# Kernel tuning notes

Hardware: AMD Instinct MI355X
Metric: run time of the kernel (lower is better)

## Reference

```python
import jax, jax.numpy as jnp
import numpy as np

N_USERS = 60000
N_ITEMS = 40000
N_NODES = N_USERS + N_ITEMS
N_EDGES = 1_000_000
D = 64
BN_EPS = 1e-3  # tf.layers.batch_normalization default epsilon


def setup_inputs() -> dict:
    key = jax.random.key(0)
    ks = jax.random.split(key, 16)
    s = 1.0 / np.sqrt(D)  # uniform-ish init scale for [D,D] weights
    w = lambda k: (jax.random.uniform(k, (D, D), jnp.float32, -1.0, 1.0) * s)
    return {
        "u_features": jax.random.normal(ks[0], (N_USERS, D), jnp.float32),
        "v_features": jax.random.normal(ks[1], (N_ITEMS, D), jnp.float32),
        "edge_start": jax.random.randint(ks[2], (N_EDGES,), 0, N_NODES, jnp.int32),
        "edge_end": jax.random.randint(ks[3], (N_EDGES,), 0, N_NODES, jnp.int32),
        "Ui1": w(ks[4]), "Uj1": w(ks[5]), "Vi1": w(ks[6]), "Vj1": w(ks[7]),
        "bu1": jnp.zeros((D,), jnp.float32), "bv1": jnp.zeros((D,), jnp.float32),
        "Ui2": w(ks[8]), "Uj2": w(ks[9]), "Vi2": w(ks[10]), "Vj2": w(ks[11]),
        "bu2": jnp.zeros((D,), jnp.float32), "bv2": jnp.zeros((D,), jnp.float32),
        "R": w(ks[12]),
        "gamma1": jnp.ones((D,), jnp.float32), "beta1": jnp.zeros((D,), jnp.float32),
        "gamma2": jnp.ones((D,), jnp.float32), "beta2": jnp.zeros((D,), jnp.float32),
    }


def _stage(x, Ui, Uj, Vi, Vj, bu, bv, e_start, e_end, n_nodes):
    # gate = sigmoid(E_end@(x Vi) + E_start@(x Vj) + bv)   -> edge gather
    gate = jax.nn.sigmoid((x @ Vi)[e_end] + (x @ Vj)[e_start] + bv)  # [E, D]
    msg = gate * (x @ Ui)[e_start]                                    # [E, D]
    # x Uj + E_end.T @ msg + bu   -> scatter-add to destination nodes
    agg = jax.ops.segment_sum(msg, e_end, num_segments=n_nodes)       # [N, D]
    return x @ Uj + agg + bu


def _batchnorm(x, gamma, beta):
    mean = jnp.mean(x, axis=0)
    var = jnp.var(x, axis=0)
    return gamma * (x - mean) * jax.lax.rsqrt(var + BN_EPS) + beta


def reference(u_features, v_features, edge_start, edge_end,
              Ui1, Uj1, Vi1, Vj1, bu1, bv1,
              Ui2, Uj2, Vi2, Vj2, bu2, bv2,
              R, gamma1, beta1, gamma2, beta2):
    num_users = u_features.shape[0]
    x_in = jnp.concatenate([u_features, v_features], axis=0)  # [N, D]
    n = x_in.shape[0]
    x = _stage(x_in, Ui1, Uj1, Vi1, Vj1, bu1, bv1, edge_start, edge_end, n)
    x = jax.nn.relu(_batchnorm(x, gamma1, beta1))
    x = _stage(x, Ui2, Uj2, Vi2, Vj2, bu2, bv2, edge_start, edge_end, n)
    x = _batchnorm(x, gamma2, beta2)
    x = jax.nn.relu(x + x_in @ R)  # residual branch
    return x[:num_users], x[num_users:]
```

## Files before the change

kernel.cpp:

```cpp
#include <hip/hip_runtime.h>
#include <hip/hip_bf16.h>

#define NUSERS 60000
#define NNODES 100000
#define DD 64
#define NGB 1563
#define GMM 782
#define NBUK 196
#define ESB 2048
#define NBH 400

typedef __hip_bfloat16 bf16;
using bf16x8 = __attribute__((ext_vector_type(8))) short;
using f32x4  = __attribute__((ext_vector_type(4))) float;

__device__ __forceinline__ float b2f(bf16 x) { return __bfloat162float(x); }
__device__ __forceinline__ bf16 f2b(float x) { return __float2bfloat16(x); }
__device__ __forceinline__ unsigned short fbits(float x) {
    union { bf16 b; unsigned short u; } cv; cv.b = f2b(x); return cv.u;
}
__device__ __forceinline__ float us2f(unsigned short h) {
    union { unsigned u; float f; } t; t.u = (unsigned)h << 16; return t.f;
}
__device__ __forceinline__ float lo_bf16(unsigned w) {
    union { unsigned u; float f; } t; t.u = w << 16; return t.f;
}
__device__ __forceinline__ float hi_bf16(unsigned w) {
    union { unsigned u; float f; } t; t.u = w & 0xFFFF0000u; return t.f;
}
__device__ __forceinline__ float ldf(const void* p, size_t i, int isbf) {
    if (isbf) return b2f(((const bf16*)p)[i]);
    return ((const float*)p)[i];
}
__device__ __forceinline__ unsigned pack2(float a, float b) {
    return (unsigned)fbits(a) | ((unsigned)fbits(b) << 16);
}
__device__ __forceinline__ unsigned pr2(float x0, float x1, float a0, float a1,
                                        float b0, float b1) {
    float t0 = a0 * x0 + b0, t1 = a1 * x1 + b1;
    t0 = t0 > 0.f ? t0 : 0.f;
    t1 = t1 > 0.f ? t1 : 0.f;
    return pack2(t0, t1);
}

__global__ __launch_bounds__(256) void k_bhist(
    const int* __restrict__ ee, const unsigned short* __restrict__ hsn,
    int* __restrict__ flag, int* __restrict__ bh, int E)
{
    __shared__ int h[256];
    int t = threadIdx.x;
    if (blockIdx.x == 0) {
        int cnt = 0;
        for (int i = t; i < 1024; i += 256) {
            int e = (hsn[2 * i] >> 7) & 0xFF;
            cnt += (e >= 100 && e <= 140) ? 1 : 0;
        }
        h[t] = cnt;
        __syncthreads();
        for (int s = 128; s > 0; s >>= 1) {
            if (t < s) h[t] += h[t + s];
            __syncthreads();
        }
        if (t == 0) flag[0] = (h[0] > 512) ? 1 : 0;
        __syncthreads();
    }
    h[t] = 0;
    __syncthreads();
    for (int e = blockIdx.x * 256 + t; e < E; e += gridDim.x * 256)
        atomicAdd(&h[ee[e] >> 9], 1);
    __syncthreads();
    bh[blockIdx.x * 256 + t] = h[t];
}

__global__ void k_bscan(const int* __restrict__ bh, int* __restrict__ bbase,
                        int* __restrict__ bcursor, float* __restrict__ redz)
{
    __shared__ int sd[256];
    int t = threadIdx.x;
    int v = 0;
    for (int b = 0; b < NBH; b++) v += bh[b * 256 + t];
    sd[t] = v;
    __syncthreads();
    for (int off = 1; off < 256; off <<= 1) {
        int x = (t >= off) ? sd[t - off] : 0;
        __syncthreads();
        sd[t] += x;
        __syncthreads();
    }
    int excl = sd[t] - v;
    bbase[t] = excl;
    bcursor[t] = excl;
    for (int i = t; i < 4096; i += 256) redz[i] = 0.f;
}

__global__ __launch_bounds__(256) void k_bscatter(
    const int* __restrict__ es, const int* __restrict__ ee,
    int* __restrict__ bcursor, unsigned* __restrict__ ebuf, int E)
{
    __shared__ int h[256], gb[256], lr[256];
    int t = threadIdx.x;
    h[t] = 0;
    lr[t] = 0;
    __syncthreads();
    int base = blockIdx.x * ESB;
    unsigned ent[8];
    int bk[8];
#pragma unroll
    for (int i = 0; i < 8; i++) {
        int e = base + t + i * 256;
        if (e < E) {
            int s = es[e], d = ee[e];
            bk[i] = d >> 9;
            ent[i] = (unsigned)s | ((unsigned)(d & 511) << 20);
            atomicAdd(&h[bk[i]], 1);
        } else bk[i] = -1;
    }
    __syncthreads();
    if (h[t]) gb[t] = atomicAdd(&bcursor[t], h[t]);
    __syncthreads();
#pragma unroll
    for (int i = 0; i < 8; i++) {
        if (bk[i] >= 0) {
            int r = atomicAdd(&lr[bk[i]], 1);
            ebuf[gb[bk[i]] + r] = ent[i];
        }
    }
}

__global__ __launch_bounds__(256) void k_group(
    const int* __restrict__ bbase, const unsigned* __restrict__ ebuf,
    int* __restrict__ rowptr, int* __restrict__ srcidx)
{
    __shared__ int h[512], sc[512];
    int b = blockIdx.x, t = threadIdx.x;
    int lo = bbase[b], hi = bbase[b + 1];
    h[t] = 0;
    h[t + 256] = 0;
    __syncthreads();
    for (int i = lo + t; i < hi; i += 256)
        atomicAdd(&h[ebuf[i] >> 20], 1);
    __syncthreads();
    sc[t] = h[t];
    sc[t + 256] = h[t + 256];
    __syncthreads();
    for (int off = 1; off < 512; off <<= 1) {
        int v0 = (t >= off) ? sc[t - off] : 0;
        int v1 = (t + 256 >= off) ? sc[t + 256 - off] : 0;
        __syncthreads();
        sc[t] += v0;
        sc[t + 256] += v1;
        __syncthreads();
    }
    int n0 = b * 512 + t, n1 = b * 512 + t + 256;
    int e0 = lo + sc[t] - h[t];
    int e1 = lo + sc[t + 256] - h[t + 256];
    if (n0 < NNODES) rowptr[n0] = e0;
    if (n1 < NNODES) rowptr[n1] = e1;
    if (b == NBUK - 1 && t == 0) rowptr[NNODES] = hi;
    h[t] = e0;
    h[t + 256] = e1;
    __syncthreads();
    for (int i = lo + t; i < hi; i += 256) {
        unsigned en = ebuf[i];
        int pos = atomicAdd(&h[en >> 20], 1);
        int s = (int)(en & 0xFFFFF);
        srcidx[pos] = s < NNODES ? s : 0;
    }
}

template <int MODE>
__device__ __forceinline__ void stage_load(
    int tile, int tid, int bfflag,
    const void* u, const void* v, const unsigned short* Aacc,
    const float* ab, uint4& w0, uint4& w1)
{
    int r = tid >> 2, c0 = (tid & 3) * 16;
    int row = tile * DD + r;
    int rowc = row < NNODES ? row : NNODES - 1;
    if (MODE == 0) {
        const void* src = (rowc < NUSERS) ? u : v;
        size_t off = (rowc < NUSERS) ? ((size_t)rowc * DD + c0)
                                     : ((size_t)(rowc - NUSERS) * DD + c0);
        if (bfflag) {
            const uint4* p = (const uint4*)((const unsigned short*)src + off);
            w0 = p[0];
            w1 = p[1];
        } else {
            const float4* p = (const float4*)((const float*)src + off);
            float4 f0 = p[0], f1 = p[1], f2 = p[2], f3 = p[3];
            w0 = make_uint4(pack2(f0.x, f0.y), pack2(f0.z, f0.w),
                            pack2(f1.x, f1.y), pack2(f1.z, f1.w));
            w1 = make_uint4(pack2(f2.x, f2.y), pack2(f2.z, f2.w),
                            pack2(f3.x, f3.y), pack2(f3.z, f3.w));
        }
    } else {
        const uint4* p = (const uint4*)(Aacc + (size_t)rowc * DD + c0);
        unsigned aw[8];
        *(uint4*)&aw[0] = p[0];
        *(uint4*)&aw[4] = p[1];
        const float4* pa = (const float4*)(ab + c0);
        const float4* pb = (const float4*)(ab + 64 + c0);
        float av[16], bv[16];
#pragma unroll
        for (int j = 0; j < 4; j++) {
            float4 fa = pa[j], fb = pb[j];
            av[4 * j] = fa.x; av[4 * j + 1] = fa.y;
            av[4 * j + 2] = fa.z; av[4 * j + 3] = fa.w;
            bv[4 * j] = fb.x; bv[4 * j + 1] = fb.y;
            bv[4 * j + 2] = fb.z; bv[4 * j + 3] = fb.w;
        }
        unsigned ow[8];
#pragma unroll
        for (int j = 0; j < 8; j++)
            ow[j] = pr2(lo_bf16(aw[j]), hi_bf16(aw[j]),
                        av[2 * j], av[2 * j + 1], bv[2 * j], bv[2 * j + 1]);
        w0 = *(uint4*)&ow[0];
        w1 = *(uint4*)&ow[4];
    }
}

__device__ __forceinline__ void stage_store(unsigned short* xbuf, int tid,
                                            const uint4& w0, const uint4& w1)
{
    int r = tid >> 2, c0 = (tid & 3) * 16;
    *(uint4*)&xbuf[r * 72 + c0] = w0;
    *((uint4*)&xbuf[r * 72 + c0] + 1) = w1;
}

template <int MODE>
__global__ __launch_bounds__(256, 4) void k_mm4_mfma(
    const void* __restrict__ u, const void* __restrict__ v,
    const float* __restrict__ red, const void* __restrict__ gm,
    const void* __restrict__ bt,
    const void* __restrict__ W0, const void* __restrict__ W1,
    const void* __restrict__ W2, const void* __restrict__ W3,
    const void* __restrict__ b0, const void* __restrict__ b1,
    const int* __restrict__ flag,
    unsigned short* __restrict__ A, unsigned short* __restrict__ Ed,
    unsigned* __restrict__ Tw)
{
    __shared__ __align__(16) unsigned short lsd[4 * DD * 72];
    __shared__ __align__(16) float abs_s[128];
    const int bfflag = flag[0];
    const int tid = threadIdx.x;

    if (MODE == 1) {
        if (tid < 64) {
            float sm = 0.f, sq = 0.f;
#pragma unroll
            for (int s = 0; s < 8; s++) {
                sm += red[s * 256 + tid];
                sq += red[s * 256 + 128 + tid];
            }
            float mean = sm * (1.f / NNODES);
            float var = sq * (1.f / NNODES) - mean * mean;
            float a = ldf(gm, tid, bfflag) * rsqrtf(var + 1e-3f);
            abs_s[tid] = a;
            abs_s[64 + tid] = ldf(bt, tid, bfflag) - mean * a;
        }
        __syncthreads();
    }

    int t = blockIdx.x;
    uint4 xa, xb;
    stage_load<MODE>(t, tid, bfflag, u, v, A, abs_s, xa, xb);

    if (bfflag) {
#define WSTG_BF(m, src)                                                   \
        _Pragma("unroll")                                                 \
        for (int j = 0; j < 2; j++) {                                     \
            int i = tid + j * 256; int e0 = i * 8;                        \
            *(uint4*)&lsd[(m) * 4608 + (e0 >> 6) * 72 + (e0 & 63)] =      \
                ((const uint4*)(src))[i];                                 \
        }
        WSTG_BF(0, W0) WSTG_BF(1, W1) WSTG_BF(2, W2) WSTG_BF(3, W3)
    } else {
#define WSTG_F32(m, src)                                                  \
        _Pragma("unroll")                                                 \
        for (int j = 0; j < 4; j++) {                                     \
            int i = tid + j * 256; int e0 = i * 4;                        \
            float4 f = ((const float4*)(src))[i];                         \
            *(uint2*)&lsd[(m) * 4608 + (e0 >> 6) * 72 + (e0 & 63)] =      \
                make_uint2(pack2(f.x, f.y), pack2(f.z, f.w));             \
        }
        WSTG_F32(0, W0) WSTG_F32(1, W1) WSTG_F32(2, W2) WSTG_F32(3, W3)
    }
    __syncthreads();

    const int wv = tid >> 6, lane = tid & 63;
    const int quad = lane >> 4, ln = lane & 15;
    const int mA = (wv < 2) ? wv : 2;
    bf16x8 bfrA[2][4], bfrB[2][4];
#pragma unroll
    for (int ks = 0; ks < 2; ks++)
#pragma unroll
        for (int nt = 0; nt < 4; nt++)
#pragma unroll
            for (int j = 0; j < 8; j++)
                bfrA[ks][nt][j] = (short)lsd[mA * 4608 +
                    (ks * 32 + quad * 8 + j) * 72 + nt * 16 + ln];
    if (wv >= 2) {
#pragma unroll
        for (int ks = 0; ks < 2; ks++)
#pragma unroll
            for (int nt = 0; nt < 4; nt++)
#pragma unroll
                for (int j = 0; j < 8; j++)
                    bfrB[ks][nt][j] = (short)lsd[3 * 4608 +
                        (ks * 32 + quad * 8 + j) * 72 + nt * 16 + ln];
    }
    float bias[4];
#pragma unroll
    for (int nt = 0; nt < 4; nt++)
        bias[nt] = (wv == 0) ? ldf(b0, nt * 16 + ln, bfflag)
                 : (wv == 1) ? ldf(b1, nt * 16 + ln, bfflag) : 0.f;
    __syncthreads();

    auto compute = [&](const unsigned short* xt, int row0) {
        if (wv < 2) {
#pragma unroll
            for (int rt = 0; rt < 4; rt++) {
                int m = rt * 16 + ln;
                bf16x8 af0 = *(const bf16x8*)&xt[m * 72 + quad * 8];
                bf16x8 af1 = *(const bf16x8*)&xt[m * 72 + 32 + quad * 8];
#pragma unroll
                for (int nt = 0; nt < 4; nt++) {
                    f32x4 c = {0.f, 0.f, 0.f, 0.f};
                    c = __builtin_amdgcn_mfma_f32_16x16x32_bf16(af0, bfrA[0][nt], c, 0, 0, 0);
                    c = __builtin_amdgcn_mfma_f32_16x16x32_bf16(af1, bfrA[1][nt], c, 0, 0, 0);
                    int col = nt * 16 + ln;
#pragma unroll
                    for (int r = 0; r < 4; r++) {
                        int row = row0 + rt * 16 + quad * 4 + r;
                        if (row < NNODES) {
                            size_t o = (size_t)row * DD + col;
                            if (wv == 0) A[o] = fbits(c[r] + bias[nt]);
                            else         Ed[o] = fbits(__expf(-(c[r] + bias[nt])));
                        }
                    }
                }
            }
        } else {
            const int rtb = (wv - 2) * 2;
#pragma unroll
            for (int rr = 0; rr < 2; rr++) {
                int rt = rtb + rr;
                int m = rt * 16 + ln;
                bf16x8 af0 = *(const bf16x8*)&xt[m * 72 + quad * 8];
                bf16x8 af1 = *(const bf16x8*)&xt[m * 72 + 32 + quad * 8];
#pragma unroll
                for (int nt = 0; nt < 4; nt++) {
                    f32x4 c2 = {0.f, 0.f, 0.f, 0.f};
                    f32x4 c3 = {0.f, 0.f, 0.f, 0.f};
                    c2 = __builtin_amdgcn_mfma_f32_16x16x32_bf16(af0, bfrA[0][nt], c2, 0, 0, 0);
                    c2 = __builtin_amdgcn_mfma_f32_16x16x32_bf16(af1, bfrA[1][nt], c2, 0, 0, 0);
                    c3 = __builtin_amdgcn_mfma_f32_16x16x32_bf16(af0, bfrB[0][nt], c3, 0, 0, 0);
                    c3 = __builtin_amdgcn_mfma_f32_16x16x32_bf16(af1, bfrB[1][nt], c3, 0, 0, 0);
                    int col = nt * 16 + ln;
#pragma unroll
                    for (int r = 0; r < 4; r++) {
                        int row = row0 + rt * 16 + quad * 4 + r;
                        if (row < NNODES)
                            Tw[(size_t)row * DD + col] =
                                pack2(c2[r], __expf(-c3[r]));
                    }
                }
            }
        }
    };

    stage_store(lsd, tid, xa, xb);
    int tn = t + GMM;
    if (tn < NGB)
        stage_load<MODE>(tn, tid, bfflag, u, v, A, abs_s, xa, xb);
    __syncthreads();
    int buf = 0;
    while (true) {
        compute(lsd + buf * 4608, t * DD);
        if (tn >= NGB) break;
        t = tn;
        tn += GMM;
        stage_store(lsd + (buf ^ 1) * 4608, tid, xa, xb);
        if (tn < NGB)
            stage_load<MODE>(tn, tid, bfflag, u, v, A, abs_s, xa, xb);
        __syncthreads();
        buf ^= 1;
    }
}

__global__ __launch_bounds__(256) void k_final_mfma(
    const unsigned short* __restrict__ A, const float* __restrict__ red,
    const void* __restrict__ gm, const void* __restrict__ bt,
    const void* __restrict__ u, const void* __restrict__ v,
    const void* __restrict__ R, const int* __restrict__ flag,
    void* __restrict__ out)
{
    __shared__ __align__(16) unsigned short Wls[DD][72];
    __shared__ __align__(16) unsigned short xls[DD][72];
    __shared__ __align__(16) float abf[128];
    const int bfflag = flag[0];
    const int tid = threadIdx.x;
    if (tid < 64) {
        float sm = 0.f, sq = 0.f;
#pragma unroll
        for (int s = 0; s < 8; s++) {
            sm += red[s * 256 + tid];
            sq += red[s * 256 + 128 + tid];
        }
        float mean = sm * (1.f / NNODES);
        float var = sq * (1.f / NNODES) - mean * mean;
        float a = ldf(gm, tid, bfflag) * rsqrtf(var + 1e-3f);
        abf[tid] = a;
        abf[64 + tid] = ldf(bt, tid, bfflag) - mean * a;
    }
    if (bfflag) {
        for (int i = tid; i < 512; i += 256) {
            int e0 = i * 8;
            *(uint4*)&Wls[e0 >> 6][e0 & 63] = ((const uint4*)R)[i];
        }
    } else {
        for (int i = tid; i < 1024; i += 256) {
            int e0 = i * 4;
            float4 f = ((const float4*)R)[i];
            *(uint2*)&Wls[e0 >> 6][e0 & 63] =
                make_uint2(pack2(f.x, f.y), pack2(f.z, f.w));
        }
    }
    uint4 w0, w1;
    stage_load<0>(blockIdx.x, tid, bfflag, u, v, nullptr, nullptr, w0, w1);
    stage_store(&xls[0][0], tid, w0, w1);
    __syncthreads();

    const int row0 = blockIdx.x * DD;
    const int wv = tid >> 6, lane = tid & 63;
    const int quad = lane >> 4, ln = lane & 15;
    bf16x8 bfr[2][4];
#pragma unroll
    for (int ks = 0; ks < 2; ks++)
#pragma unroll
        for (int nt = 0; nt < 4; nt++)
#pragma unroll
            for (int j = 0; j < 8; j++)
                bfr[ks][nt][j] = (short)Wls[ks * 32 + quad * 8 + j][nt * 16 + ln];
    float av[4], bv[4];
#pragma unroll
    for (int nt = 0; nt < 4; nt++) {
        av[nt] = abf[nt * 16 + ln];
        bv[nt] = abf[64 + nt * 16 + ln];
    }
    const int rt = wv;
    int m = rt * 16 + ln;
    bf16x8 af0 = *(const bf16x8*)&xls[m][quad * 8];
    bf16x8 af1 = *(const bf16x8*)&xls[m][32 + quad * 8];
#pragma unroll
    for (int nt = 0; nt < 4; nt++) {
        f32x4 c = {0.f, 0.f, 0.f, 0.f};
        c = __builtin_amdgcn_mfma_f32_16x16x32_bf16(af0, bfr[0][nt], c, 0, 0, 0);
        c = __builtin_amdgcn_mfma_f32_16x16x32_bf16(af1, bfr[1][nt], c, 0, 0, 0);
        int col = nt * 16 + ln;
#pragma unroll
        for (int r = 0; r < 4; r++) {
            int row = row0 + rt * 16 + quad * 4 + r;
            if (row < NNODES) {
                size_t o = (size_t)row * DD + col;
                float vv = av[nt] * us2f(A[o]) + bv[nt] + c[r];
                vv = vv > 0.f ? vv : 0.f;
                if (bfflag) ((unsigned short*)out)[o] = fbits(vv);
                else        ((float*)out)[o] = vv;
            }
        }
    }
}

__global__ __launch_bounds__(256) void k_accum(
    const int* __restrict__ rowptr, const int* __restrict__ srcidx,
    const unsigned* __restrict__ T, const bf16* __restrict__ Ed,
    unsigned short* __restrict__ A)
{
    const int wv = threadIdx.x >> 6, c = threadIdx.x & 63;
    int d1 = blockIdx.x * 8 + wv;
    int d2 = d1 + 4;
    int p0 = rowptr[d1], p1 = rowptr[d1 + 1];
    int q0 = rowptr[d2], q1 = rowptr[d2 + 1];
    size_t o1 = (size_t)d1 * DD + c, o2 = (size_t)d2 * DD + c;
    float ed1 = b2f(Ed[o1]), ed2 = b2f(Ed[o2]);
    float sum1 = us2f(A[o1]), sum2 = us2f(A[o2]);

#define EDGE(sv, edv, tv) sv += lo_bf16(tv) * \
    __builtin_amdgcn_rcpf(1.f + edv * hi_bf16(tv));
#define NODE_LOOP(sv, edv, r0, r1)                                  \
    {                                                               \
        int i = r0;                                                 \
        for (; i + 7 < r1; i += 8) {                                \
            unsigned t0 = T[(size_t)srcidx[i] * DD + c];            \
            unsigned t1 = T[(size_t)srcidx[i + 1] * DD + c];        \
            unsigned t2 = T[(size_t)srcidx[i + 2] * DD + c];        \
            unsigned t3 = T[(size_t)srcidx[i + 3] * DD + c];        \
            unsigned t4 = T[(size_t)srcidx[i + 4] * DD + c];        \
            unsigned t5 = T[(size_t)srcidx[i + 5] * DD + c];        \
            unsigned t6 = T[(size_t)srcidx[i + 6] * DD + c];        \
            unsigned t7 = T[(size_t)srcidx[i + 7] * DD + c];        \
            EDGE(sv, edv, t0) EDGE(sv, edv, t1)                     \
            EDGE(sv, edv, t2) EDGE(sv, edv, t3)                     \
            EDGE(sv, edv, t4) EDGE(sv, edv, t5)                     \
            EDGE(sv, edv, t6) EDGE(sv, edv, t7)                     \
        }                                                           \
        for (; i + 3 < r1; i += 4) {                                \
            unsigned t0 = T[(size_t)srcidx[i] * DD + c];            \
            unsigned t1 = T[(size_t)srcidx[i + 1] * DD + c];        \
            unsigned t2 = T[(size_t)srcidx[i + 2] * DD + c];        \
            unsigned t3 = T[(size_t)srcidx[i + 3] * DD + c];        \
            EDGE(sv, edv, t0) EDGE(sv, edv, t1)                     \
            EDGE(sv, edv, t2) EDGE(sv, edv, t3)                     \
        }                                                           \
        for (; i < r1; i++) {                                       \
            unsigned t0 = T[(size_t)srcidx[i] * DD + c];            \
            EDGE(sv, edv, t0)                                       \
        }                                                           \
    }

    NODE_LOOP(sum1, ed1, p0, p1)
    A[o1] = fbits(sum1);
    NODE_LOOP(sum2, ed2, q0, q1)
    A[o2] = fbits(sum2);
#undef NODE_LOOP
#undef EDGE
}

__global__ __launch_bounds__(256) void k_reduce(
    const unsigned short* __restrict__ x, float* __restrict__ red)
{
    __shared__ float s1[256], s2[256];
    const int c = threadIdx.x & 63, rg = threadIdx.x >> 6;
    float a0 = 0.f, a1 = 0.f, a2 = 0.f, a3 = 0.f;
    float q0 = 0.f, q1 = 0.f, q2 = 0.f, q3 = 0.f;
    for (int row = blockIdx.x * 16 + rg * 4; row < NNODES;
         row += gridDim.x * 16) {
        float v0 = us2f(x[(size_t)row * DD + c]);
        float v1 = (row + 1 < NNODES) ? us2f(x[(size_t)(row + 1) * DD + c]) : 0.f;
        float v2 = (row + 2 < NNODES) ? us2f(x[(size_t)(row + 2) * DD + c]) : 0.f;
        float v3 = (row + 3 < NNODES) ? us2f(x[(size_t)(row + 3) * DD + c]) : 0.f;
        a0 += v0; q0 += v0 * v0;
        a1 += v1; q1 += v1 * v1;
        a2 += v2; q2 += v2 * v2;
        a3 += v3; q3 += v3 * v3;
    }
    s1[threadIdx.x] = (a0 + a1) + (a2 + a3);
    s2[threadIdx.x] = (q0 + q1) + (q2 + q3);
    __syncthreads();
    if (threadIdx.x < 64) {
        float sum = s1[c] + s1[64 + c] + s1[128 + c] + s1[192 + c];
        float sq = s2[c] + s2[64 + c] + s2[128 + c] + s2[192 + c];
        float* sh = red + (blockIdx.x & 7) * 256;
        unsafeAtomicAdd(&sh[c], sum);
        unsafeAtomicAdd(&sh[128 + c], sq);
    }
}

extern "C" void kernel_launch(void* const* d_in, const int* in_sizes, int n_in,
                              void* d_out, int out_size, void* d_ws, size_t ws_size,
                              hipStream_t stream)
{
    const void* u   = d_in[0];
    const void* v   = d_in[1];
    const int* es   = (const int*)d_in[2];
    const int* ee   = (const int*)d_in[3];
    const void* Ui1 = d_in[4];
    const void* Uj1 = d_in[5];
    const void* Vi1 = d_in[6];
    const void* Vj1 = d_in[7];
    const void* bu1 = d_in[8];
    const void* bv1 = d_in[9];
    const void* Ui2 = d_in[10];
    const void* Uj2 = d_in[11];
    const void* Vi2 = d_in[12];
    const void* Vj2 = d_in[13];
    const void* bu2 = d_in[14];
    const void* bv2 = d_in[15];
    const void* R   = d_in[16];
    const void* g1  = d_in[17];
    const void* be1 = d_in[18];
    const void* g2  = d_in[19];
    const void* be2 = d_in[20];
    const int E = in_sizes[2];

    char* ws = (char*)d_ws;
    unsigned short* A = (unsigned short*)(ws);
    unsigned* T    = (unsigned*)(ws + 25600000);
    unsigned* ebuf = (unsigned*)(ws + 25600000);
    int* srcidx    = (int*)(ws + 51200000);
    int* bh        = (int*)(ws + 51200000);
    float* redsh   = (float*)(ws + 55200000);
    int* rowptr    = (int*)(ws + 56000000);
    int* flag      = (int*)(ws + 56804224);
    int* bbase     = (int*)(ws + 56805376);
    int* bcursor   = (int*)(ws + 56806400);
    float* red1 = redsh;
    float* red2 = redsh + 2048;
    bf16* Ed = (bf16*)d_out;

    k_bhist<<<NBH, 256, 0, stream>>>(ee, (const unsigned short*)u, flag, bh, E);
    k_bscan<<<1, 256, 0, stream>>>(bh, bbase, bcursor, redsh);
    k_bscatter<<<(E + ESB - 1) / ESB, 256, 0, stream>>>(es, ee, bcursor, ebuf, E);
    k_group<<<NBUK, 256, 0, stream>>>(bbase, ebuf, rowptr, srcidx);

    k_mm4_mfma<0><<<GMM, 256, 0, stream>>>(u, v, nullptr, nullptr, nullptr,
                                           Uj1, Vi1, Ui1, Vj1, bu1, bv1, flag,
                                           A, (unsigned short*)Ed, T);
    k_accum<<<NNODES / 8, 256, 0, stream>>>(rowptr, srcidx, T, Ed, A);
    k_reduce<<<1024, 256, 0, stream>>>(A, red1);

    k_mm4_mfma<1><<<GMM, 256, 0, stream>>>(nullptr, nullptr, red1, g1, be1,
                                           Uj2, Vi2, Ui2, Vj2, bu2, bv2, flag,
                                           A, (unsigned short*)Ed, T);
    k_accum<<<NNODES / 8, 256, 0, stream>>>(rowptr, srcidx, T, Ed, A);
    k_reduce<<<1024, 256, 0, stream>>>(A, red2);

    k_final_mfma<<<NGB, 256, 0, stream>>>(A, red2, g2, be2, u, v, R, flag, d_out);
}
```

Before: 345.0 us.

## Fuse BN statistics into accumulation and stage MFMA outputs through LDS

Drops the separate k_reduce passes. k_accum now accumulates each block's per-column sum and sum of squares and adds them atomically into 64 shards instead of 8, which avoids re-reading the 100000x64 activation twice. The MFMA kernels (k_mm4_mfma and k_final_mfma) now stage results in shared memory and write full rows with 16-byte stores, replacing scattered 2-byte stores. In exchange there are extra syncthreads and LDS traffic, 64 shards to sum per block, and the statistics are taken from fp32 values before bf16 rounding.

```diff
diff --git a/kernel.cpp b/kernel.cpp
--- a/kernel.cpp
+++ b/kernel.cpp
@@ -9,6 +9,7 @@
 #define NBUK 196
 #define ESB 2048
 #define NBH 400
+#define NSH 64
 
 typedef __hip_bfloat16 bf16;
 using bf16x8 = __attribute__((ext_vector_type(8))) short;
@@ -90,7 +91,7 @@
     int excl = sd[t] - v;
     bbase[t] = excl;
     bcursor[t] = excl;
-    for (int i = t; i < 4096; i += 256) redz[i] = 0.f;
+    for (int i = t; i < 2 * NSH * 256; i += 256) redz[i] = 0.f;
 }
 
 __global__ __launch_bounds__(256) void k_bscatter(
@@ -247,8 +248,8 @@
     if (MODE == 1) {
         if (tid < 64) {
             float sm = 0.f, sq = 0.f;
-#pragma unroll
-            for (int s = 0; s < 8; s++) {
+#pragma unroll 8
+            for (int s = 0; s < NSH; s++) {
                 sm += red[s * 256 + tid];
                 sq += red[s * 256 + 128 + tid];
             }
@@ -318,6 +319,7 @@
 
     auto compute = [&](const unsigned short* xt, int row0) {
         if (wv < 2) {
+            unsigned short* stg = lsd + (2 + wv) * 4608;
 #pragma unroll
             for (int rt = 0; rt < 4; rt++) {
                 int m = rt * 16 + ln;
@@ -328,17 +330,24 @@
                     f32x4 c = {0.f, 0.f, 0.f, 0.f};
                     c = __builtin_amdgcn_mfma_f32_16x16x32_bf16(af0, bfrA[0][nt], c, 0, 0, 0);
                     c = __builtin_amdgcn_mfma_f32_16x16x32_bf16(af1, bfrA[1][nt], c, 0, 0, 0);
-                    int col = nt * 16 + ln;
 #pragma unroll
                     for (int r = 0; r < 4; r++) {
-                        int row = row0 + rt * 16 + quad * 4 + r;
-                        if (row < NNODES) {
-                            size_t o = (size_t)row * DD + col;
-                            if (wv == 0) A[o] = fbits(c[r] + bias[nt]);
-                            else         Ed[o] = fbits(__expf(-(c[r] + bias[nt])));
-                        }
+                        int lr = rt * 16 + quad * 4 + r;
+                        float vv = c[r] + bias[nt];
+                        stg[lr * 72 + nt * 16 + ln] =
+                            (wv == 0) ? fbits(vv) : fbits(__expf(-vv));
                     }
                 }
+            }
+            unsigned short* dst = (wv == 0) ? A : Ed;
+            int r8 = lane >> 3, c8 = lane & 7;
+#pragma unroll
+            for (int p = 0; p < 8; p++) {
+                int lr = p * 8 + r8;
+                uint4 vv = *(const uint4*)&stg[lr * 72 + c8 * 8];
+                int row = row0 + lr;
+                if (row < NNODES)
+                    *(uint4*)&dst[(size_t)row * DD + c8 * 8] = vv;
             }
         } else {
             const int rtb = (wv - 2) * 2;
@@ -402,8 +411,8 @@
     const int tid = threadIdx.x;
     if (tid < 64) {
         float sm = 0.f, sq = 0.f;
-#pragma unroll
-        for (int s = 0; s < 8; s++) {
+#pragma unroll 8
+        for (int s = 0; s < NSH; s++) {
             sm += red[s * 256 + tid];
             sq += red[s * 256 + 128 + tid];
         }
@@ -452,6 +461,7 @@
     int m = rt * 16 + ln;
     bf16x8 af0 = *(const bf16x8*)&xls[m][quad * 8];
     bf16x8 af1 = *(const bf16x8*)&xls[m][32 + quad * 8];
+    __syncthreads();
 #pragma unroll
     for (int nt = 0; nt < 4; nt++) {
         f32x4 c = {0.f, 0.f, 0.f, 0.f};
@@ -465,9 +475,21 @@
                 size_t o = (size_t)row * DD + col;
                 float vv = av[nt] * us2f(A[o]) + bv[nt] + c[r];
                 vv = vv > 0.f ? vv : 0.f;
-                if (bfflag) ((unsigned short*)out)[o] = fbits(vv);
+                if (bfflag) Wls[rt * 16 + quad * 4 + r][col] = fbits(vv);
                 else        ((float*)out)[o] = vv;
             }
+        }
+    }
+    if (bfflag) {
+        __syncthreads();
+#pragma unroll
+        for (int p = 0; p < 2; p++) {
+            int ci = p * 256 + tid;
+            int lr = ci >> 3, c8 = ci & 7;
+            int row = row0 + lr;
+            uint4 vv = *(const uint4*)&Wls[lr][c8 * 8];
+            if (row < NNODES)
+                *(uint4*)&((unsigned short*)out)[(size_t)row * DD + c8 * 8] = vv;
         }
     }
 }
@@ -475,8 +497,9 @@
 __global__ __launch_bounds__(256) void k_accum(
     const int* __restrict__ rowptr, const int* __restrict__ srcidx,
     const unsigned* __restrict__ T, const bf16* __restrict__ Ed,
-    unsigned short* __restrict__ A)
-{
+    unsigned short* __restrict__ A, float* __restrict__ red)
+{
+    __shared__ float s1[256], s2[256];
     const int wv = threadIdx.x >> 6, c = threadIdx.x & 63;
     int d1 = blockIdx.x * 8 + wv;
     int d2 = d1 + 4;
@@ -525,35 +548,16 @@
     A[o2] = fbits(sum2);
 #undef NODE_LOOP
 #undef EDGE
-}
-
-__global__ __launch_bounds__(256) void k_reduce(
-    const unsigned short* __restrict__ x, float* __restrict__ red)
-{
-    __shared__ float s1[256], s2[256];
-    const int c = threadIdx.x & 63, rg = threadIdx.x >> 6;
-    float a0 = 0.f, a1 = 0.f, a2 = 0.f, a3 = 0.f;
-    float q0 = 0.f, q1 = 0.f, q2 = 0.f, q3 = 0.f;
-    for (int row = blockIdx.x * 16 + rg * 4; row < NNODES;
-         row += gridDim.x * 16) {
-        float v0 = us2f(x[(size_t)row * DD + c]);
-        float v1 = (row + 1 < NNODES) ? us2f(x[(size_t)(row + 1) * DD + c]) : 0.f;
-        float v2 = (row + 2 < NNODES) ? us2f(x[(size_t)(row + 2) * DD + c]) : 0.f;
-        float v3 = (row + 3 < NNODES) ? us2f(x[(size_t)(row + 3) * DD + c]) : 0.f;
-        a0 += v0; q0 += v0 * v0;
-        a1 += v1; q1 += v1 * v1;
-        a2 += v2; q2 += v2 * v2;
-        a3 += v3; q3 += v3 * v3;
-    }
-    s1[threadIdx.x] = (a0 + a1) + (a2 + a3);
-    s2[threadIdx.x] = (q0 + q1) + (q2 + q3);
+
+    s1[threadIdx.x] = sum1 + sum2;
+    s2[threadIdx.x] = sum1 * sum1 + sum2 * sum2;
     __syncthreads();
     if (threadIdx.x < 64) {
-        float sum = s1[c] + s1[64 + c] + s1[128 + c] + s1[192 + c];
-        float sq = s2[c] + s2[64 + c] + s2[128 + c] + s2[192 + c];
-        float* sh = red + (blockIdx.x & 7) * 256;
-        unsafeAtomicAdd(&sh[c], sum);
-        unsafeAtomicAdd(&sh[128 + c], sq);
+        float a = s1[c] + s1[64 + c] + s1[128 + c] + s1[192 + c];
+        float b = s2[c] + s2[64 + c] + s2[128 + c] + s2[192 + c];
+        float* sh = red + (blockIdx.x & (NSH - 1)) * 256;
+        unsafeAtomicAdd(&sh[c], a);
+        unsafeAtomicAdd(&sh[128 + c], b);
     }
 }
 
@@ -596,7 +600,7 @@
     int* bbase     = (int*)(ws + 56805376);
     int* bcursor   = (int*)(ws + 56806400);
     float* red1 = redsh;
-    float* red2 = redsh + 2048;
+    float* red2 = redsh + NSH * 256;
     bf16* Ed = (bf16*)d_out;
 
     k_bhist<<<NBH, 256, 0, stream>>>(ee, (const unsigned short*)u, flag, bh, E);
@@ -607,14 +611,12 @@
     k_mm4_mfma<0><<<GMM, 256, 0, stream>>>(u, v, nullptr, nullptr, nullptr,
                                            Uj1, Vi1, Ui1, Vj1, bu1, bv1, flag,
                                            A, (unsigned short*)Ed, T);
-    k_accum<<<NNODES / 8, 256, 0, stream>>>(rowptr, srcidx, T, Ed, A);
-    k_reduce<<<1024, 256, 0, stream>>>(A, red1);
+    k_accum<<<NNODES / 8, 256, 0, stream>>>(rowptr, srcidx, T, Ed, A, red1);
 
     k_mm4_mfma<1><<<GMM, 256, 0, stream>>>(nullptr, nullptr, red1, g1, be1,
                                            Uj2, Vi2, Ui2, Vj2, bu2, bv2, flag,
                                            A, (unsigned short*)Ed, T);
-    k_accum<<<NNODES / 8, 256, 0, stream>>>(rowptr, srcidx, T, Ed, A);
-    k_reduce<<<1024, 256, 0, stream>>>(A, red2);
+    k_accum<<<NNODES / 8, 256, 0, stream>>>(rowptr, srcidx, T, Ed, A, red2);
 
     k_final_mfma<<<NGB, 256, 0, stream>>>(A, red2, g2, be2, u, v, R, flag, d_out);
 }
```

After: 339.9 us. Within noise of the previous version (-1.5%).
